# Performance work log

Hardware: AMD Instinct MI355X
Metric: run time of the kernel (lower is better)

Reference implementation:

```python
import jax, jax.numpy as jnp
import numpy as np

B, SEQ, IN, H = 256, 128, 512, 512


def setup_inputs() -> dict:
    key = jax.random.key(0)
    ks = jax.random.split(key, 7)
    s = 1.0 / np.sqrt(H)  # torch LSTM/Linear default init scale
    return {
        "x": jax.random.normal(ks[0], (B, SEQ, IN), dtype=jnp.float32),
        "W_ih": jax.random.uniform(ks[1], (4 * H, IN), jnp.float32, -s, s),
        "W_hh": jax.random.uniform(ks[2], (4 * H, H), jnp.float32, -s, s),
        "b_ih": jax.random.uniform(ks[3], (4 * H,), jnp.float32, -s, s),
        "b_hh": jax.random.uniform(ks[4], (4 * H,), jnp.float32, -s, s),
        "Wa": jax.random.uniform(ks[5], (SEQ, H), jnp.float32, -s, s),
        "ba": jax.random.uniform(ks[6], (SEQ,), jnp.float32, -s, s),
    }


def _lstm_cell(xi, h, c, W_ih, W_hh, b):
    # torch gate order: input, forget, cell(g), output
    gates = xi @ W_ih.T + h @ W_hh.T + b  # [B, 4H]
    i, f, g, o = jnp.split(gates, 4, axis=-1)
    c_new = jax.nn.sigmoid(f) * c + jax.nn.sigmoid(i) * jnp.tanh(g)
    h_new = jax.nn.sigmoid(o) * jnp.tanh(c_new)
    return h_new, c_new


def reference(x, W_ih, W_hh, b_ih, b_hh, Wa, ba):
    b = b_ih + b_hh
    bs, seq = x.shape[0], Wa.shape[0]
    h = jnp.zeros((bs, W_hh.shape[1]), x.dtype)
    c = jnp.zeros_like(h)
    # initial step on zero input (x[:,0]*0), zero initial state
    h, c = _lstm_cell(jnp.zeros((bs, x.shape[2]), x.dtype), h, c, W_ih, W_hh, b)

    def step(carry, _):
        h, c = carry
        attn = jax.nn.softmax(c @ Wa.T + ba, axis=-1)      # [B, seq]
        xi = jnp.einsum('bs,bsd->bd', attn, x)             # attention-weighted input
        h, c = _lstm_cell(xi, h, c, W_ih, W_hh, b)
        return (h, c), h

    _, hs = jax.lax.scan(step, (h, c), None, length=seq)   # [seq, B, H]
    return jnp.transpose(hs, (1, 0, 2))                    # [B, seq, H]
```

## Files before the change

### kernel.cpp

```cpp
#include <hip/hip_runtime.h>
#include <stdint.h>

#define BDIM 256
#define SEQL 128
#define IND 512
#define HID 512
#define KDIM 1024

typedef __bf16 bf16x8 __attribute__((ext_vector_type(8)));
typedef float floatx4 __attribute__((ext_vector_type(4)));
typedef _Float16 f16x8 __attribute__((ext_vector_type(8)));

__device__ __forceinline__ float sigm(float x) { return 1.0f / (1.0f + __expf(-x)); }

__device__ __forceinline__ ushort f2bf(float v) {
  uint32_t x = __builtin_bit_cast(uint32_t, v);
  x += 0x7fffu + ((x >> 16) & 1u);
  return (ushort)(x >> 16);
}
__device__ __forceinline__ float bf2f(ushort u) {
  return __builtin_bit_cast(float, ((uint32_t)u) << 16);
}

__global__ __launch_bounds__(256) void k_wconv(
    const float* __restrict__ W_ih, const float* __restrict__ W_hh,
    const float* __restrict__ b_ih, const float* __restrict__ b_hh,
    ushort* __restrict__ Whi, ushort* __restrict__ Wlo, float* __restrict__ bias) {
  int row = blockIdx.x;
  if (threadIdx.x == 0) bias[row] = b_ih[row] + b_hh[row];
  for (int k = threadIdx.x; k < KDIM; k += 256) {
    float w = (k < IND) ? W_ih[(size_t)row * IND + k] : W_hh[(size_t)row * HID + (k - IND)];
    ushort hi = f2bf(w);
    Whi[(size_t)row * KDIM + k] = hi;
    Wlo[(size_t)row * KDIM + k] = f2bf(w - bf2f(hi));
  }
}

__global__ __launch_bounds__(256) void k_xconv(const float* __restrict__ x,
                                               _Float16* __restrict__ xh) {
  size_t i = ((size_t)blockIdx.x * 256 + threadIdx.x) * 8;
  float4 v0 = *(const float4*)(x + i);
  float4 v1 = *(const float4*)(x + i + 4);
  f16x8 o;
  o[0] = (_Float16)v0.x; o[1] = (_Float16)v0.y; o[2] = (_Float16)v0.z; o[3] = (_Float16)v0.w;
  o[4] = (_Float16)v1.x; o[5] = (_Float16)v1.y; o[6] = (_Float16)v1.z; o[7] = (_Float16)v1.w;
  *(f16x8*)(xh + i) = o;
}

__global__ void k_init(const float* __restrict__ b_ih, const float* __restrict__ b_hh,
                       float* __restrict__ c, ushort* __restrict__ Ahi, ushort* __restrict__ Alo) {
  int b = blockIdx.x;
  for (int j = threadIdx.x; j < HID; j += blockDim.x) {
    float bi = b_ih[j] + b_hh[j];
    float bg = b_ih[2 * HID + j] + b_hh[2 * HID + j];
    float bo = b_ih[3 * HID + j] + b_hh[3 * HID + j];
    float c0 = sigm(bi) * tanhf(bg);
    float h0 = sigm(bo) * tanhf(c0);
    c[b * HID + j] = c0;
    ushort hi = f2bf(h0);
    Ahi[(size_t)b * KDIM + IND + j] = hi;
    Alo[(size_t)b * KDIM + IND + j] = f2bf(h0 - bf2f(hi));
  }
}

struct AttnS { float sc[HID]; float sl[SEQL]; float sxi[4][HID]; };
struct GateS {
  ushort sA[2][2][16][72];
  ushort sW[2][2][2][64][72];
  float  sR[2][4][16][16];
};
union SU { AttnS a; GateS g; };

__device__ __forceinline__ void gsync(unsigned* cnt, unsigned target) {
  __syncthreads();
  if (threadIdx.x == 0) {
    __hip_atomic_fetch_add(cnt, 1u, __ATOMIC_RELEASE, __HIP_MEMORY_SCOPE_AGENT);
    while (__hip_atomic_load(cnt, __ATOMIC_RELAXED, __HIP_MEMORY_SCOPE_AGENT) < target)
      __builtin_amdgcn_s_sleep(4);
    (void)__hip_atomic_load(cnt, __ATOMIC_ACQUIRE, __HIP_MEMORY_SCOPE_AGENT);
  }
  __syncthreads();
}

#define MLOAD(R, KO) do { \
  R##a   = *(const uint4*)(gA + (KO)); \
  R##w00 = *(const uint4*)(gW0hi + (KO)); R##w01 = *(const uint4*)(gW0hi + (KO) + 8); \
  R##w02 = *(const uint4*)(gW0lo + (KO)); R##w03 = *(const uint4*)(gW0lo + (KO) + 8); \
  R##w10 = *(const uint4*)(gW1hi + (KO)); R##w11 = *(const uint4*)(gW1hi + (KO) + 8); \
  R##w12 = *(const uint4*)(gW1lo + (KO)); R##w13 = *(const uint4*)(gW1lo + (KO) + 8); } while (0)
#define MSTORE(BUF, R) do { \
  *(uint4*)&su.g.sA[BUF][sthalf][ar][ac] = R##a; \
  *(uint4*)&su.g.sW[BUF][0][0][wr][wc] = R##w00; *(uint4*)&su.g.sW[BUF][0][0][wr][wc + 8] = R##w01; \
  *(uint4*)&su.g.sW[BUF][0][1][wr][wc] = R##w02; *(uint4*)&su.g.sW[BUF][0][1][wr][wc + 8] = R##w03; \
  *(uint4*)&su.g.sW[BUF][1][0][wr][wc] = R##w10; *(uint4*)&su.g.sW[BUF][1][0][wr][wc + 8] = R##w11; \
  *(uint4*)&su.g.sW[BUF][1][1][wr][wc] = R##w12; *(uint4*)&su.g.sW[BUF][1][1][wr][wc + 8] = R##w13; } while (0)
#define MCOMPUTE(BUF) do { \
  _Pragma("unroll") for (int ks = 0; ks < 2; ++ks) { \
    int kb = ks * 32 + koff; \
    bf16x8 ah = *(const bf16x8*)(&su.g.sA[BUF][0][ml][kb]); \
    bf16x8 al = *(const bf16x8*)(&su.g.sA[BUF][1][ml][kb]); \
    bf16x8 wh0 = *(const bf16x8*)(&su.g.sW[BUF][0][0][g * 16 + ml][kb]); \
    bf16x8 wl0 = *(const bf16x8*)(&su.g.sW[BUF][0][1][g * 16 + ml][kb]); \
    bf16x8 wh1 = *(const bf16x8*)(&su.g.sW[BUF][1][0][g * 16 + ml][kb]); \
    bf16x8 wl1 = *(const bf16x8*)(&su.g.sW[BUF][1][1][g * 16 + ml][kb]); \
    acc0A = __builtin_amdgcn_mfma_f32_16x16x32_bf16(ah, wh0, acc0A, 0, 0, 0); \
    acc1A = __builtin_amdgcn_mfma_f32_16x16x32_bf16(ah, wh1, acc1A, 0, 0, 0); \
    acc0B = __builtin_amdgcn_mfma_f32_16x16x32_bf16(ah, wl0, acc0B, 0, 0, 0); \
    acc0B = __builtin_amdgcn_mfma_f32_16x16x32_bf16(al, wh0, acc0B, 0, 0, 0); \
    acc1B = __builtin_amdgcn_mfma_f32_16x16x32_bf16(ah, wl1, acc1B, 0, 0, 0); \
    acc1B = __builtin_amdgcn_mfma_f32_16x16x32_bf16(al, wh1, acc1B, 0, 0, 0); } } while (0)

__global__ __launch_bounds__(256) void k_step(
    float* __restrict__ c, const float* __restrict__ Wa,
    const float* __restrict__ ba, const _Float16* __restrict__ xh,
    const ushort* __restrict__ Whi, const ushort* __restrict__ Wlo,
    const float* __restrict__ bias,
    const ushort* __restrict__ Rhi, const ushort* __restrict__ Rlo,
    ushort* __restrict__ Dhi, ushort* __restrict__ Dlo,
    float* __restrict__ out, unsigned* __restrict__ bar, int t) {
  __shared__ __align__(16) SU su;
  int blk = blockIdx.x, tid = threadIdx.x;
  int lane = tid & 63, wave = tid >> 6;
  int n = blk & 7, s = blk >> 3;
  int bt = s & 15, psel = s >> 4;
  int b0 = bt * 16;
  int myb = b0 + 2 * n + psel;
  int j0a = (4 * n + 2 * psel) * 16;
  int j0b = j0a + 16;

  {
    su.a.sc[tid] = c[myb * HID + tid];
    su.a.sc[tid + 256] = c[myb * HID + tid + 256];
    __syncthreads();
    float4 c0 = *(const float4*)(&su.a.sc[lane * 4]);
    float4 c1 = *(const float4*)(&su.a.sc[lane * 4 + 256]);
#pragma unroll 4
    for (int si = 0; si < 32; ++si) {
      int ss = wave * 32 + si;
      const float4* wr4 = (const float4*)(Wa + (size_t)ss * HID);
      float4 w0 = wr4[lane];
      float4 w1 = wr4[lane + 64];
      float acc = c0.x * w0.x + c0.y * w0.y + c0.z * w0.z + c0.w * w0.w
                + c1.x * w1.x + c1.y * w1.y + c1.z * w1.z + c1.w * w1.w;
#pragma unroll
      for (int off = 32; off > 0; off >>= 1) acc += __shfl_down(acc, off);
      if (lane == 0) su.a.sl[ss] = acc + ba[ss];
    }
    __syncthreads();
    if (tid < 64) {
      float v0 = su.a.sl[tid], v1 = su.a.sl[tid + 64];
      float m = fmaxf(v0, v1);
#pragma unroll
      for (int off = 32; off > 0; off >>= 1) m = fmaxf(m, __shfl_xor(m, off));
      float e0 = __expf(v0 - m), e1 = __expf(v1 - m);
      float s2 = e0 + e1;
#pragma unroll
      for (int off = 32; off > 0; off >>= 1) s2 += __shfl_xor(s2, off);
      float inv = 1.f / s2;
      su.a.sl[tid] = e0 * inv; su.a.sl[tid + 64] = e1 * inv;
    }
    __syncthreads();
    int cix = tid & 63, qp = tid >> 6;
    const _Float16* xrow = xh + (size_t)myb * SEQL * IND + (size_t)qp * 32 * IND + 8 * cix;
    float a0 = 0.f, a1 = 0.f, a2 = 0.f, a3 = 0.f, a4 = 0.f, a5 = 0.f, a6 = 0.f, a7 = 0.f;
#pragma unroll 8
    for (int ss = 0; ss < 32; ++ss) {
      float w = su.a.sl[qp * 32 + ss];
      f16x8 v = *(const f16x8*)(xrow + (size_t)ss * IND);
      a0 += w * (float)v[0]; a1 += w * (float)v[1];
      a2 += w * (float)v[2]; a3 += w * (float)v[3];
      a4 += w * (float)v[4]; a5 += w * (float)v[5];
      a6 += w * (float)v[6]; a7 += w * (float)v[7];
    }
    *(float4*)(&su.a.sxi[qp][8 * cix])     = (float4){a0, a1, a2, a3};
    *(float4*)(&su.a.sxi[qp][8 * cix + 4]) = (float4){a4, a5, a6, a7};
    __syncthreads();
    float rx = su.a.sxi[0][2 * tid] + su.a.sxi[1][2 * tid] + su.a.sxi[2][2 * tid] + su.a.sxi[3][2 * tid];
    float ry = su.a.sxi[0][2 * tid + 1] + su.a.sxi[1][2 * tid + 1] + su.a.sxi[2][2 * tid + 1] + su.a.sxi[3][2 * tid + 1];
    ushort hx = f2bf(rx), hy = f2bf(ry);
    uint hp = (uint)hx | ((uint)hy << 16);
    uint lp = (uint)f2bf(rx - bf2f(hx)) | ((uint)f2bf(ry - bf2f(hy)) << 16);
    *(uint*)(const_cast<ushort*>(Rhi) + (size_t)myb * KDIM + 2 * tid) = hp;
    *(uint*)(const_cast<ushort*>(Rlo) + (size_t)myb * KDIM + 2 * tid) = lp;
  }

  gsync(bar + bt * 16, 16u * (unsigned)(t + 1));

  {
    int sthalf = tid >> 7;
    int ar = (tid & 127) >> 3, ac = (tid & 7) * 8;
    const ushort* gA = (sthalf ? Rlo : Rhi) + (size_t)(b0 + ar) * KDIM + ac;
    int wr = tid >> 2, wc = (tid & 3) * 16;
    int wrow0 = (wr >> 4) * HID + j0a + (wr & 15);
    const ushort* gW0hi = Whi + (size_t)wrow0 * KDIM + wc;
    const ushort* gW0lo = Wlo + (size_t)wrow0 * KDIM + wc;
    const ushort* gW1hi = Whi + (size_t)(wrow0 + 16) * KDIM + wc;
    const ushort* gW1lo = Wlo + (size_t)(wrow0 + 16) * KDIM + wc;

    floatx4 acc0A = {0.f, 0.f, 0.f, 0.f}, acc0B = {0.f, 0.f, 0.f, 0.f};
    floatx4 acc1A = {0.f, 0.f, 0.f, 0.f}, acc1B = {0.f, 0.f, 0.f, 0.f};
    int g = tid >> 6, ml = lane & 15, koff = (lane >> 4) * 8;

    uint4 Aa, Aw00, Aw01, Aw02, Aw03, Aw10, Aw11, Aw12, Aw13;
    uint4 Ba, Bw00, Bw01, Bw02, Bw03, Bw10, Bw11, Bw12, Bw13;

    MLOAD(A, 0);
    MLOAD(B, 64);
    MSTORE(0, A);
    MSTORE(1, B);
    MLOAD(A, 128);
    MLOAD(B, 192);
    __syncthreads();

    for (int k0 = 0; k0 < 16; k0 += 2) {
      MCOMPUTE(0);
      __syncthreads();
      if (k0 + 2 < 16) {
        MSTORE(0, A);
        if (k0 + 4 < 16) MLOAD(A, (k0 + 4) * 64);
      }
      MCOMPUTE(1);
      __syncthreads();
      if (k0 + 3 < 16) {
        MSTORE(1, B);
        if (k0 + 5 < 16) MLOAD(B, (k0 + 5) * 64);
      }
    }

    {
      floatx4 r0 = acc0A + acc0B, r1 = acc1A + acc1B;
#pragma unroll
      for (int r = 0; r < 4; ++r) {
        su.g.sR[0][g][ml][(lane >> 4) * 4 + r] = r0[r];
        su.g.sR[1][g][ml][(lane >> 4) * 4 + r] = r1[r];
      }
    }
    __syncthreads();

    int jj = tid & 15, bb = tid >> 4;
#pragma unroll
    for (int t2 = 0; t2 < 2; ++t2) {
      int jg = (t2 ? j0b : j0a) + jj;
      int b = b0 + bb;
      float ig = sigm(su.g.sR[t2][0][jj][bb] + bias[jg]);
      float fg = sigm(su.g.sR[t2][1][jj][bb] + bias[HID + jg]);
      float gg = tanhf(su.g.sR[t2][2][jj][bb] + bias[2 * HID + jg]);
      float og = sigm(su.g.sR[t2][3][jj][bb] + bias[3 * HID + jg]);
      float co = c[b * HID + jg];
      float cn = fg * co + ig * gg;
      float hv = og * tanhf(cn);
      c[b * HID + jg] = cn;
      out[((size_t)b * SEQL + t) * HID + jg] = hv;
      ushort hi = f2bf(hv);
      Dhi[(size_t)b * KDIM + IND + jg] = hi;
      Dlo[(size_t)b * KDIM + IND + jg] = f2bf(hv - bf2f(hi));
    }
  }
}

extern "C" void kernel_launch(void* const* d_in, const int* in_sizes, int n_in,
                              void* d_out, int out_size, void* d_ws, size_t ws_size,
                              hipStream_t stream) {
  (void)in_sizes; (void)n_in; (void)out_size; (void)ws_size;
  const float* x    = (const float*)d_in[0];
  const float* W_ih = (const float*)d_in[1];
  const float* W_hh = (const float*)d_in[2];
  const float* b_ih = (const float*)d_in[3];
  const float* b_hh = (const float*)d_in[4];
  const float* Wa   = (const float*)d_in[5];
  const float* ba   = (const float*)d_in[6];
  float* out = (float*)d_out;

  char* p = (char*)d_ws;
  auto carve = [&](size_t bytes) { char* r = p; p += (bytes + 255) & ~(size_t)255; return r; };
  unsigned* bar = (unsigned*)carve(1024);
  float*  c    = (float*)carve((size_t)BDIM * HID * 4);
  float*  bias = (float*)carve((size_t)4 * HID * 4);
  ushort* Whi  = (ushort*)carve((size_t)4 * HID * KDIM * 2);
  ushort* Wlo  = (ushort*)carve((size_t)4 * HID * KDIM * 2);
  ushort* A0hi = (ushort*)carve((size_t)BDIM * KDIM * 2);
  ushort* A0lo = (ushort*)carve((size_t)BDIM * KDIM * 2);
  ushort* A1hi = (ushort*)carve((size_t)BDIM * KDIM * 2);
  ushort* A1lo = (ushort*)carve((size_t)BDIM * KDIM * 2);
  _Float16* xh = (_Float16*)carve((size_t)BDIM * SEQL * IND * 2);

  hipMemsetAsync(bar, 0, 1024, stream);
  k_wconv<<<4 * HID, 256, 0, stream>>>(W_ih, W_hh, b_ih, b_hh, Whi, Wlo, bias);
  k_xconv<<<(BDIM * SEQL * IND) / (256 * 8), 256, 0, stream>>>(x, xh);
  k_init<<<BDIM, 256, 0, stream>>>(b_ih, b_hh, c, A0hi, A0lo);

  for (int t = 0; t < SEQL; ++t) {
    ushort* Rhi = (t & 1) ? A1hi : A0hi;
    ushort* Rlo = (t & 1) ? A1lo : A0lo;
    ushort* Dhi = (t & 1) ? A0hi : A1hi;
    ushort* Dlo = (t & 1) ? A0lo : A1lo;
    k_step<<<256, 256, 0, stream>>>(c, Wa, ba, xh, Whi, Wlo, bias,
                                    Rhi, Rlo, Dhi, Dlo, out, bar, t);
  }
}
```

Measured before the change: 5.175 ms.

## Fuse per-timestep launches into one persistent kernel with x cached in LDS

Replaces 128 per-step launches with a single persistent kernel of 256 blocks. Each block loops over time and uses group atomic barriers between the attention phase and the gate GEMM, and again at the end of each step. Each block converts its batch row of x to fp16 once and keeps it in shared memory (128KB), which removes the separate conversion kernel and the per-step global reads of x. The gate GEMM now runs as two sequential single-buffered 16-column passes instead of one double-buffered pass. This saves launch overhead but adds barrier cost, lowers occupancy because of the large LDS footprint, and exposes more load latency. It also relies on all 256 blocks being co-resident.

```diff
diff --git a/kernel.cpp b/kernel.cpp
--- a/kernel.cpp
+++ b/kernel.cpp
@@ -34,17 +34,6 @@
     Whi[(size_t)row * KDIM + k] = hi;
     Wlo[(size_t)row * KDIM + k] = f2bf(w - bf2f(hi));
   }
-}
-
-__global__ __launch_bounds__(256) void k_xconv(const float* __restrict__ x,
-                                               _Float16* __restrict__ xh) {
-  size_t i = ((size_t)blockIdx.x * 256 + threadIdx.x) * 8;
-  float4 v0 = *(const float4*)(x + i);
-  float4 v1 = *(const float4*)(x + i + 4);
-  f16x8 o;
-  o[0] = (_Float16)v0.x; o[1] = (_Float16)v0.y; o[2] = (_Float16)v0.z; o[3] = (_Float16)v0.w;
-  o[4] = (_Float16)v1.x; o[5] = (_Float16)v1.y; o[6] = (_Float16)v1.z; o[7] = (_Float16)v1.w;
-  *(f16x8*)(xh + i) = o;
 }
 
 __global__ void k_init(const float* __restrict__ b_ih, const float* __restrict__ b_hh,
@@ -63,62 +52,53 @@
   }
 }
 
-struct AttnS { float sc[HID]; float sl[SEQL]; float sxi[4][HID]; };
-struct GateS {
-  ushort sA[2][2][16][72];
-  ushort sW[2][2][2][64][72];
-  float  sR[2][4][16][16];
+struct __align__(16) StepS {
+  _Float16 sx[SEQL][IND];
+  union {
+    struct { float sl[SEQL]; float sxi[4][HID]; } a;
+    struct { ushort sA[2][16][72]; ushort sW[2][64][72]; float sR[4][16][16]; } g;
+  } u;
 };
-union SU { AttnS a; GateS g; };
 
 __device__ __forceinline__ void gsync(unsigned* cnt, unsigned target) {
   __syncthreads();
   if (threadIdx.x == 0) {
     __hip_atomic_fetch_add(cnt, 1u, __ATOMIC_RELEASE, __HIP_MEMORY_SCOPE_AGENT);
     while (__hip_atomic_load(cnt, __ATOMIC_RELAXED, __HIP_MEMORY_SCOPE_AGENT) < target)
-      __builtin_amdgcn_s_sleep(4);
+      __builtin_amdgcn_s_sleep(2);
     (void)__hip_atomic_load(cnt, __ATOMIC_ACQUIRE, __HIP_MEMORY_SCOPE_AGENT);
   }
   __syncthreads();
 }
 
-#define MLOAD(R, KO) do { \
-  R##a   = *(const uint4*)(gA + (KO)); \
-  R##w00 = *(const uint4*)(gW0hi + (KO)); R##w01 = *(const uint4*)(gW0hi + (KO) + 8); \
-  R##w02 = *(const uint4*)(gW0lo + (KO)); R##w03 = *(const uint4*)(gW0lo + (KO) + 8); \
-  R##w10 = *(const uint4*)(gW1hi + (KO)); R##w11 = *(const uint4*)(gW1hi + (KO) + 8); \
-  R##w12 = *(const uint4*)(gW1lo + (KO)); R##w13 = *(const uint4*)(gW1lo + (KO) + 8); } while (0)
-#define MSTORE(BUF, R) do { \
-  *(uint4*)&su.g.sA[BUF][sthalf][ar][ac] = R##a; \
-  *(uint4*)&su.g.sW[BUF][0][0][wr][wc] = R##w00; *(uint4*)&su.g.sW[BUF][0][0][wr][wc + 8] = R##w01; \
-  *(uint4*)&su.g.sW[BUF][0][1][wr][wc] = R##w02; *(uint4*)&su.g.sW[BUF][0][1][wr][wc + 8] = R##w03; \
-  *(uint4*)&su.g.sW[BUF][1][0][wr][wc] = R##w10; *(uint4*)&su.g.sW[BUF][1][0][wr][wc + 8] = R##w11; \
-  *(uint4*)&su.g.sW[BUF][1][1][wr][wc] = R##w12; *(uint4*)&su.g.sW[BUF][1][1][wr][wc + 8] = R##w13; } while (0)
-#define MCOMPUTE(BUF) do { \
+#define SBLOAD(KO) do { \
+  Pa  = *(const uint4*)(gA + (KO)); \
+  Pw0 = *(const uint4*)(gWhi + (KO)); Pw1 = *(const uint4*)(gWhi + (KO) + 8); \
+  Pw2 = *(const uint4*)(gWlo + (KO)); Pw3 = *(const uint4*)(gWlo + (KO) + 8); } while (0)
+#define SBSTORE() do { \
+  *(uint4*)&S.u.g.sA[sthalf][ar][ac] = Pa; \
+  *(uint4*)&S.u.g.sW[0][wr][wc] = Pw0; *(uint4*)&S.u.g.sW[0][wr][wc + 8] = Pw1; \
+  *(uint4*)&S.u.g.sW[1][wr][wc] = Pw2; *(uint4*)&S.u.g.sW[1][wr][wc + 8] = Pw3; } while (0)
+#define SBCOMPUTE() do { \
   _Pragma("unroll") for (int ks = 0; ks < 2; ++ks) { \
     int kb = ks * 32 + koff; \
-    bf16x8 ah = *(const bf16x8*)(&su.g.sA[BUF][0][ml][kb]); \
-    bf16x8 al = *(const bf16x8*)(&su.g.sA[BUF][1][ml][kb]); \
-    bf16x8 wh0 = *(const bf16x8*)(&su.g.sW[BUF][0][0][g * 16 + ml][kb]); \
-    bf16x8 wl0 = *(const bf16x8*)(&su.g.sW[BUF][0][1][g * 16 + ml][kb]); \
-    bf16x8 wh1 = *(const bf16x8*)(&su.g.sW[BUF][1][0][g * 16 + ml][kb]); \
-    bf16x8 wl1 = *(const bf16x8*)(&su.g.sW[BUF][1][1][g * 16 + ml][kb]); \
-    acc0A = __builtin_amdgcn_mfma_f32_16x16x32_bf16(ah, wh0, acc0A, 0, 0, 0); \
-    acc1A = __builtin_amdgcn_mfma_f32_16x16x32_bf16(ah, wh1, acc1A, 0, 0, 0); \
-    acc0B = __builtin_amdgcn_mfma_f32_16x16x32_bf16(ah, wl0, acc0B, 0, 0, 0); \
-    acc0B = __builtin_amdgcn_mfma_f32_16x16x32_bf16(al, wh0, acc0B, 0, 0, 0); \
-    acc1B = __builtin_amdgcn_mfma_f32_16x16x32_bf16(ah, wl1, acc1B, 0, 0, 0); \
-    acc1B = __builtin_amdgcn_mfma_f32_16x16x32_bf16(al, wh1, acc1B, 0, 0, 0); } } while (0)
-
-__global__ __launch_bounds__(256) void k_step(
-    float* __restrict__ c, const float* __restrict__ Wa,
-    const float* __restrict__ ba, const _Float16* __restrict__ xh,
+    bf16x8 ah = *(const bf16x8*)(&S.u.g.sA[0][ml][kb]); \
+    bf16x8 al = *(const bf16x8*)(&S.u.g.sA[1][ml][kb]); \
+    bf16x8 wh = *(const bf16x8*)(&S.u.g.sW[0][g * 16 + ml][kb]); \
+    bf16x8 wl = *(const bf16x8*)(&S.u.g.sW[1][g * 16 + ml][kb]); \
+    accA = __builtin_amdgcn_mfma_f32_16x16x32_bf16(ah, wh, accA, 0, 0, 0); \
+    accB = __builtin_amdgcn_mfma_f32_16x16x32_bf16(ah, wl, accB, 0, 0, 0); \
+    accB = __builtin_amdgcn_mfma_f32_16x16x32_bf16(al, wh, accB, 0, 0, 0); } } while (0)
+
+__global__ __launch_bounds__(256) void k_persist(
+    const float* __restrict__ x, const float* __restrict__ Wa,
+    const float* __restrict__ ba, float* __restrict__ c,
     const ushort* __restrict__ Whi, const ushort* __restrict__ Wlo,
     const float* __restrict__ bias,
-    const ushort* __restrict__ Rhi, const ushort* __restrict__ Rlo,
-    ushort* __restrict__ Dhi, ushort* __restrict__ Dlo,
-    float* __restrict__ out, unsigned* __restrict__ bar, int t) {
-  __shared__ __align__(16) SU su;
+    ushort* __restrict__ A0hi, ushort* __restrict__ A0lo,
+    ushort* __restrict__ A1hi, ushort* __restrict__ A1lo,
+    float* __restrict__ out, unsigned* __restrict__ bar) {
+  __shared__ StepS S;
   int blk = blockIdx.x, tid = threadIdx.x;
   int lane = tid & 63, wave = tid >> 6;
   int n = blk & 7, s = blk >> 3;
@@ -126,135 +106,130 @@
   int b0 = bt * 16;
   int myb = b0 + 2 * n + psel;
   int j0a = (4 * n + 2 * psel) * 16;
-  int j0b = j0a + 16;
+  unsigned* gcnt = bar + bt * 16;
 
   {
-    su.a.sc[tid] = c[myb * HID + tid];
-    su.a.sc[tid + 256] = c[myb * HID + tid + 256];
-    __syncthreads();
-    float4 c0 = *(const float4*)(&su.a.sc[lane * 4]);
-    float4 c1 = *(const float4*)(&su.a.sc[lane * 4 + 256]);
+    const float* xb = x + (size_t)myb * SEQL * IND;
+    _Float16* sxf = &S.sx[0][0];
+    for (int i = 0; i < 32; ++i) {
+      size_t o = (size_t)i * 2048 + (size_t)tid * 8;
+      float4 v0 = *(const float4*)(xb + o);
+      float4 v1 = *(const float4*)(xb + o + 4);
+      f16x8 h;
+      h[0] = (_Float16)v0.x; h[1] = (_Float16)v0.y; h[2] = (_Float16)v0.z; h[3] = (_Float16)v0.w;
+      h[4] = (_Float16)v1.x; h[5] = (_Float16)v1.y; h[6] = (_Float16)v1.z; h[7] = (_Float16)v1.w;
+      *(f16x8*)(sxf + o) = h;
+    }
+  }
+  __syncthreads();
+
+  int sthalf = tid >> 7;
+  int ar = (tid & 127) >> 3, ac = (tid & 7) * 8;
+  int wr = tid >> 2, wc = (tid & 3) * 16;
+  int g = tid >> 6, ml = lane & 15, koff = (lane >> 4) * 8;
+  int jj = tid & 15, bb = tid >> 4;
+
+  for (int t = 0; t < SEQL; ++t) {
+    ushort* Rhi = (t & 1) ? A1hi : A0hi;
+    ushort* Rlo = (t & 1) ? A1lo : A0lo;
+    ushort* Dhi = (t & 1) ? A0hi : A1hi;
+    ushort* Dlo = (t & 1) ? A0lo : A1lo;
+
+    {
+      float4 c0 = *(const float4*)(c + (size_t)myb * HID + lane * 4);
+      float4 c1 = *(const float4*)(c + (size_t)myb * HID + lane * 4 + 256);
 #pragma unroll 4
-    for (int si = 0; si < 32; ++si) {
-      int ss = wave * 32 + si;
-      const float4* wr4 = (const float4*)(Wa + (size_t)ss * HID);
-      float4 w0 = wr4[lane];
-      float4 w1 = wr4[lane + 64];
-      float acc = c0.x * w0.x + c0.y * w0.y + c0.z * w0.z + c0.w * w0.w
-                + c1.x * w1.x + c1.y * w1.y + c1.z * w1.z + c1.w * w1.w;
-#pragma unroll
-      for (int off = 32; off > 0; off >>= 1) acc += __shfl_down(acc, off);
-      if (lane == 0) su.a.sl[ss] = acc + ba[ss];
+      for (int si = 0; si < 32; ++si) {
+        int ss = wave * 32 + si;
+        const float4* wr4 = (const float4*)(Wa + (size_t)ss * HID);
+        float4 w0 = wr4[lane];
+        float4 w1 = wr4[lane + 64];
+        float acc = c0.x * w0.x + c0.y * w0.y + c0.z * w0.z + c0.w * w0.w
+                  + c1.x * w1.x + c1.y * w1.y + c1.z * w1.z + c1.w * w1.w;
+#pragma unroll
+        for (int off = 32; off > 0; off >>= 1) acc += __shfl_down(acc, off);
+        if (lane == 0) S.u.a.sl[ss] = acc + ba[ss];
+      }
+      __syncthreads();
+      if (tid < 64) {
+        float v0 = S.u.a.sl[tid], v1 = S.u.a.sl[tid + 64];
+        float m = fmaxf(v0, v1);
+#pragma unroll
+        for (int off = 32; off > 0; off >>= 1) m = fmaxf(m, __shfl_xor(m, off));
+        float e0 = __expf(v0 - m), e1 = __expf(v1 - m);
+        float s2 = e0 + e1;
+#pragma unroll
+        for (int off = 32; off > 0; off >>= 1) s2 += __shfl_xor(s2, off);
+        float inv = 1.f / s2;
+        S.u.a.sl[tid] = e0 * inv; S.u.a.sl[tid + 64] = e1 * inv;
+      }
+      __syncthreads();
+      int cix = tid & 63, qp = tid >> 6;
+      const _Float16* xrow = &S.sx[qp * 32][8 * cix];
+      float a0 = 0.f, a1 = 0.f, a2 = 0.f, a3 = 0.f, a4 = 0.f, a5 = 0.f, a6 = 0.f, a7 = 0.f;
+#pragma unroll 8
+      for (int ss = 0; ss < 32; ++ss) {
+        float w = S.u.a.sl[qp * 32 + ss];
+        f16x8 v = *(const f16x8*)(xrow + (size_t)ss * IND);
+        a0 += w * (float)v[0]; a1 += w * (float)v[1];
+        a2 += w * (float)v[2]; a3 += w * (float)v[3];
+        a4 += w * (float)v[4]; a5 += w * (float)v[5];
+        a6 += w * (float)v[6]; a7 += w * (float)v[7];
+      }
+      *(float4*)(&S.u.a.sxi[qp][8 * cix])     = (float4){a0, a1, a2, a3};
+      *(float4*)(&S.u.a.sxi[qp][8 * cix + 4]) = (float4){a4, a5, a6, a7};
+      __syncthreads();
+      float rx = S.u.a.sxi[0][2 * tid] + S.u.a.sxi[1][2 * tid] + S.u.a.sxi[2][2 * tid] + S.u.a.sxi[3][2 * tid];
+      float ry = S.u.a.sxi[0][2 * tid + 1] + S.u.a.sxi[1][2 * tid + 1] + S.u.a.sxi[2][2 * tid + 1] + S.u.a.sxi[3][2 * tid + 1];
+      ushort hx = f2bf(rx), hy = f2bf(ry);
+      uint hp = (uint)hx | ((uint)hy << 16);
+      uint lp = (uint)f2bf(rx - bf2f(hx)) | ((uint)f2bf(ry - bf2f(hy)) << 16);
+      *(uint*)(Rhi + (size_t)myb * KDIM + 2 * tid) = hp;
+      *(uint*)(Rlo + (size_t)myb * KDIM + 2 * tid) = lp;
     }
-    __syncthreads();
-    if (tid < 64) {
-      float v0 = su.a.sl[tid], v1 = su.a.sl[tid + 64];
-      float m = fmaxf(v0, v1);
-#pragma unroll
-      for (int off = 32; off > 0; off >>= 1) m = fmaxf(m, __shfl_xor(m, off));
-      float e0 = __expf(v0 - m), e1 = __expf(v1 - m);
-      float s2 = e0 + e1;
-#pragma unroll
-      for (int off = 32; off > 0; off >>= 1) s2 += __shfl_xor(s2, off);
-      float inv = 1.f / s2;
-      su.a.sl[tid] = e0 * inv; su.a.sl[tid + 64] = e1 * inv;
+    gsync(gcnt, 32u * (unsigned)t + 16u);
+
+#pragma unroll 1
+    for (int t2 = 0; t2 < 2; ++t2) {
+      int j0 = j0a + 16 * t2;
+      const ushort* gA = (sthalf ? Rlo : Rhi) + (size_t)(b0 + ar) * KDIM + ac;
+      int wrow = (wr >> 4) * HID + j0 + (wr & 15);
+      const ushort* gWhi = Whi + (size_t)wrow * KDIM + wc;
+      const ushort* gWlo = Wlo + (size_t)wrow * KDIM + wc;
+      floatx4 accA = {0.f, 0.f, 0.f, 0.f}, accB = {0.f, 0.f, 0.f, 0.f};
+      uint4 Pa, Pw0, Pw1, Pw2, Pw3;
+      SBLOAD(0);
+      for (int k0 = 0; k0 < 16; ++k0) {
+        SBSTORE();
+        __syncthreads();
+        if (k0 + 1 < 16) SBLOAD((k0 + 1) * 64);
+        SBCOMPUTE();
+        __syncthreads();
+      }
+      {
+        floatx4 acc = accA + accB;
+#pragma unroll
+        for (int r = 0; r < 4; ++r) S.u.g.sR[g][ml][(lane >> 4) * 4 + r] = acc[r];
+      }
+      __syncthreads();
+      {
+        int jg = j0 + jj, b = b0 + bb;
+        float ig = sigm(S.u.g.sR[0][jj][bb] + bias[jg]);
+        float fg = sigm(S.u.g.sR[1][jj][bb] + bias[HID + jg]);
+        float gg = tanhf(S.u.g.sR[2][jj][bb] + bias[2 * HID + jg]);
+        float og = sigm(S.u.g.sR[3][jj][bb] + bias[3 * HID + jg]);
+        float co = c[(size_t)b * HID + jg];
+        float cn = fg * co + ig * gg;
+        float hv = og * tanhf(cn);
+        c[(size_t)b * HID + jg] = cn;
+        out[((size_t)b * SEQL + t) * HID + jg] = hv;
+        ushort hi = f2bf(hv);
+        Dhi[(size_t)b * KDIM + IND + jg] = hi;
+        Dlo[(size_t)b * KDIM + IND + jg] = f2bf(hv - bf2f(hi));
+      }
+      __syncthreads();
     }
-    __syncthreads();
-    int cix = tid & 63, qp = tid >> 6;
-    const _Float16* xrow = xh + (size_t)myb * SEQL * IND + (size_t)qp * 32 * IND + 8 * cix;
-    float a0 = 0.f, a1 = 0.f, a2 = 0.f, a3 = 0.f, a4 = 0.f, a5 = 0.f, a6 = 0.f, a7 = 0.f;
-#pragma unroll 8
-    for (int ss = 0; ss < 32; ++ss) {
-      float w = su.a.sl[qp * 32 + ss];
-      f16x8 v = *(const f16x8*)(xrow + (size_t)ss * IND);
-      a0 += w * (float)v[0]; a1 += w * (float)v[1];
-      a2 += w * (float)v[2]; a3 += w * (float)v[3];
-      a4 += w * (float)v[4]; a5 += w * (float)v[5];
-      a6 += w * (float)v[6]; a7 += w * (float)v[7];
-    }
-    *(float4*)(&su.a.sxi[qp][8 * cix])     = (float4){a0, a1, a2, a3};
-    *(float4*)(&su.a.sxi[qp][8 * cix + 4]) = (float4){a4, a5, a6, a7};
-    __syncthreads();
-    float rx = su.a.sxi[0][2 * tid] + su.a.sxi[1][2 * tid] + su.a.sxi[2][2 * tid] + su.a.sxi[3][2 * tid];
-    float ry = su.a.sxi[0][2 * tid + 1] + su.a.sxi[1][2 * tid + 1] + su.a.sxi[2][2 * tid + 1] + su.a.sxi[3][2 * tid + 1];
-    ushort hx = f2bf(rx), hy = f2bf(ry);
-    uint hp = (uint)hx | ((uint)hy << 16);
-    uint lp = (uint)f2bf(rx - bf2f(hx)) | ((uint)f2bf(ry - bf2f(hy)) << 16);
-    *(uint*)(const_cast<ushort*>(Rhi) + (size_t)myb * KDIM + 2 * tid) = hp;
-    *(uint*)(const_cast<ushort*>(Rlo) + (size_t)myb * KDIM + 2 * tid) = lp;
-  }
-
-  gsync(bar + bt * 16, 16u * (unsigned)(t + 1));
-
-  {
-    int sthalf = tid >> 7;
-    int ar = (tid & 127) >> 3, ac = (tid & 7) * 8;
-    const ushort* gA = (sthalf ? Rlo : Rhi) + (size_t)(b0 + ar) * KDIM + ac;
-    int wr = tid >> 2, wc = (tid & 3) * 16;
-    int wrow0 = (wr >> 4) * HID + j0a + (wr & 15);
-    const ushort* gW0hi = Whi + (size_t)wrow0 * KDIM + wc;
-    const ushort* gW0lo = Wlo + (size_t)wrow0 * KDIM + wc;
-    const ushort* gW1hi = Whi + (size_t)(wrow0 + 16) * KDIM + wc;
-    const ushort* gW1lo = Wlo + (size_t)(wrow0 + 16) * KDIM + wc;
-
-    floatx4 acc0A = {0.f, 0.f, 0.f, 0.f}, acc0B = {0.f, 0.f, 0.f, 0.f};
-    floatx4 acc1A = {0.f, 0.f, 0.f, 0.f}, acc1B = {0.f, 0.f, 0.f, 0.f};
-    int g = tid >> 6, ml = lane & 15, koff = (lane >> 4) * 8;
-
-    uint4 Aa, Aw00, Aw01, Aw02, Aw03, Aw10, Aw11, Aw12, Aw13;
-    uint4 Ba, Bw00, Bw01, Bw02, Bw03, Bw10, Bw11, Bw12, Bw13;
-
-    MLOAD(A, 0);
-    MLOAD(B, 64);
-    MSTORE(0, A);
-    MSTORE(1, B);
-    MLOAD(A, 128);
-    MLOAD(B, 192);
-    __syncthreads();
-
-    for (int k0 = 0; k0 < 16; k0 += 2) {
-      MCOMPUTE(0);
-      __syncthreads();
-      if (k0 + 2 < 16) {
-        MSTORE(0, A);
-        if (k0 + 4 < 16) MLOAD(A, (k0 + 4) * 64);
-      }
-      MCOMPUTE(1);
-      __syncthreads();
-      if (k0 + 3 < 16) {
-        MSTORE(1, B);
-        if (k0 + 5 < 16) MLOAD(B, (k0 + 5) * 64);
-      }
-    }
-
-    {
-      floatx4 r0 = acc0A + acc0B, r1 = acc1A + acc1B;
-#pragma unroll
-      for (int r = 0; r < 4; ++r) {
-        su.g.sR[0][g][ml][(lane >> 4) * 4 + r] = r0[r];
-        su.g.sR[1][g][ml][(lane >> 4) * 4 + r] = r1[r];
-      }
-    }
-    __syncthreads();
-
-    int jj = tid & 15, bb = tid >> 4;
-#pragma unroll
-    for (int t2 = 0; t2 < 2; ++t2) {
-      int jg = (t2 ? j0b : j0a) + jj;
-      int b = b0 + bb;
-      float ig = sigm(su.g.sR[t2][0][jj][bb] + bias[jg]);
-      float fg = sigm(su.g.sR[t2][1][jj][bb] + bias[HID + jg]);
-      float gg = tanhf(su.g.sR[t2][2][jj][bb] + bias[2 * HID + jg]);
-      float og = sigm(su.g.sR[t2][3][jj][bb] + bias[3 * HID + jg]);
-      float co = c[b * HID + jg];
-      float cn = fg * co + ig * gg;
-      float hv = og * tanhf(cn);
-      c[b * HID + jg] = cn;
-      out[((size_t)b * SEQL + t) * HID + jg] = hv;
-      ushort hi = f2bf(hv);
-      Dhi[(size_t)b * KDIM + IND + jg] = hi;
-      Dlo[(size_t)b * KDIM + IND + jg] = f2bf(hv - bf2f(hi));
-    }
+    gsync(gcnt, 32u * (unsigned)t + 32u);
   }
 }
 
@@ -282,19 +257,10 @@
   ushort* A0lo = (ushort*)carve((size_t)BDIM * KDIM * 2);
   ushort* A1hi = (ushort*)carve((size_t)BDIM * KDIM * 2);
   ushort* A1lo = (ushort*)carve((size_t)BDIM * KDIM * 2);
-  _Float16* xh = (_Float16*)carve((size_t)BDIM * SEQL * IND * 2);
 
   hipMemsetAsync(bar, 0, 1024, stream);
   k_wconv<<<4 * HID, 256, 0, stream>>>(W_ih, W_hh, b_ih, b_hh, Whi, Wlo, bias);
-  k_xconv<<<(BDIM * SEQL * IND) / (256 * 8), 256, 0, stream>>>(x, xh);
   k_init<<<BDIM, 256, 0, stream>>>(b_ih, b_hh, c, A0hi, A0lo);
-
-  for (int t = 0; t < SEQL; ++t) {
-    ushort* Rhi = (t & 1) ? A1hi : A0hi;
-    ushort* Rlo = (t & 1) ? A1lo : A0lo;
-    ushort* Dhi = (t & 1) ? A0hi : A1hi;
-    ushort* Dlo = (t & 1) ? A0lo : A1lo;
-    k_step<<<256, 256, 0, stream>>>(c, Wa, ba, xh, Whi, Wlo, bias,
-                                    Rhi, Rlo, Dhi, Dlo, out, bar, t);
-  }
-}
+  k_persist<<<BDIM, 256, 0, stream>>>(x, Wa, ba, c, Whi, Wlo, bias,
+                                      A0hi, A0lo, A1hi, A1lo, out, bar);
+}
```

Measured after the change: 6.318 ms. 22.1% more time.
